# Kernel tuning notes

Measured on AMD Instinct MI355X. Metric: run time of the kernel, lower is better.

Reference implementation:

```python
import jax, jax.numpy as jnp
import numpy as np

N_NODES = 100000
N_EDGES = 1200000
N_FEAT = 128
HIDDEN = 64
N_CLASSES = 40


def setup_inputs() -> dict:
    key = jax.random.key(0)
    k1, k2, k3, k4 = jax.random.split(key, 4)
    x = jax.random.normal(k1, (N_NODES, N_FEAT), dtype=jnp.float32)
    edge_index = jax.random.randint(k2, (2, N_EDGES), 0, N_NODES, dtype=jnp.int64)
    # Glorot-style init for the linear weights (as in PyG GCNConv)
    W1 = jax.random.normal(k3, (N_FEAT, HIDDEN), dtype=jnp.float32) * (1.0 / np.sqrt(N_FEAT))
    b1 = jnp.zeros((HIDDEN,), dtype=jnp.float32)
    W2 = jax.random.normal(k4, (HIDDEN, N_CLASSES), dtype=jnp.float32) * (1.0 / np.sqrt(HIDDEN))
    b2 = jnp.zeros((N_CLASSES,), dtype=jnp.float32)
    return {"x": x, "edge_index": edge_index, "W1": W1, "b1": b1, "W2": W2, "b2": b2}


def _gcn_conv(x, row, col, dinv, W, b):
    # x: [N, Fin], W: [Fin, Fout]. Transform then normalized scatter-add aggregation.
    h = x @ W                                  # [N, Fout]
    norm = dinv[row] * dinv[col]               # [E'] symmetric normalization
    msgs = h[row] * norm[:, None]              # [E', Fout] gather + scale
    out = jax.ops.segment_sum(msgs, col, num_segments=x.shape[0])  # scatter-add
    return out + b


def reference(x, edge_index, W1, b1, W2, b2):
    N = x.shape[0]
    loops = jnp.arange(N, dtype=edge_index.dtype)
    # add self loops (PyG GCNConv default)
    row = jnp.concatenate([edge_index[0], loops])
    col = jnp.concatenate([edge_index[1], loops])
    deg = jax.ops.segment_sum(jnp.ones_like(col, dtype=x.dtype), col, num_segments=N)
    dinv = jax.lax.rsqrt(deg)  # deg >= 1 thanks to self loops
    h = jax.nn.relu(_gcn_conv(x, row, col, dinv, W1, b1))
    # dropout is identity at inference (training=False)
    return _gcn_conv(h, row, col, dinv, W2, b2)
```

## Files before the change

### kernel.cpp

```cpp
#include <hip/hip_runtime.h>
#include <hip/hip_fp16.h>
#include <type_traits>

#define N_NODES 100000
#define N_EDGES 1200000
#define N_FEAT 128
#define HIDDEN 64
#define N_CLASSES 40

#define BSHIFT 9
#define BMASK 511
#define BUCKET_NODES 512
#define NBK ((N_NODES + BUCKET_NODES - 1) / BUCKET_NODES)
#define BCAP 8192
#define CHUNK 2048

typedef _Float16 f16x8 __attribute__((ext_vector_type(8)));
typedef float f32x4 __attribute__((ext_vector_type(4)));


__global__ __launch_bounds__(256) void bucket_kernel(const int* __restrict__ row,
                                                     const int* __restrict__ col,
                                                     int* __restrict__ gcursor,
                                                     unsigned* __restrict__ bke, int E) {
    __shared__ int hist[NBK];
    __shared__ int pfx[NBK];
    __shared__ int gbase[NBK];
    __shared__ int lcnt[NBK];
    __shared__ unsigned ord[CHUNK];
    __shared__ unsigned char obkt[CHUNK];

    const int t = threadIdx.x;
    const int e0 = blockIdx.x * CHUNK;
    const int nE = min(CHUNK, E - e0);

    for (int i = t; i < NBK; i += 256) {
        hist[i] = 0;
        lcnt[i] = 0;
    }
    __syncthreads();

    for (int i = t; i < nE; i += 256) atomicAdd(&hist[col[e0 + i] >> BSHIFT], 1);
    __syncthreads();

    int v = (t < NBK) ? hist[t] : 0;
    if (t < NBK) pfx[t] = v;
    __syncthreads();
    for (int d = 1; d < 256; d <<= 1) {
        int add = (t >= d && t < NBK) ? pfx[t - d] : 0;
        __syncthreads();
        if (t < NBK) pfx[t] += add;
        __syncthreads();
    }
    if (t < NBK) {
        pfx[t] -= v;
        gbase[t] = t * BCAP + ((v > 0) ? atomicAdd(&gcursor[t], v) : 0);
    }
    __syncthreads();

    for (int i = t; i < nE; i += 256) {
        int r = row[e0 + i];
        int c = col[e0 + i];
        int b = c >> BSHIFT;
        int pos = pfx[b] + atomicAdd(&lcnt[b], 1);
        ord[pos] = ((unsigned)r << BSHIFT) | (unsigned)(c & BMASK);
        obkt[pos] = (unsigned char)b;
    }
    __syncthreads();

    for (int i = t; i < nE; i += 256) {
        int b = obkt[i];
        bke[(size_t)gbase[b] + (i - pfx[b])] = ord[i];
    }
}


__global__ __launch_bounds__(256) void place_kernel(const int* __restrict__ gcursor,
                                                    const unsigned* __restrict__ bke,
                                                    int* __restrict__ rowptr,
                                                    float* __restrict__ dinv,
                                                    int* __restrict__ csr_src, int n) {
    __shared__ int hist[BUCKET_NODES];
    __shared__ int cur[BUCKET_NODES];
    __shared__ int tsum[256];

    const int b = blockIdx.x, t = threadIdx.x;
    const int node0 = b << BSHIFT;
    const int nNodes = min(BUCKET_NODES, n - node0);

    const int myCnt = (t < NBK) ? gcursor[t] : 0;
    tsum[t] = myCnt;
    __syncthreads();
    for (int d = 1; d < 256; d <<= 1) {
        int add = (t >= d) ? tsum[t - d] : 0;
        __syncthreads();
        tsum[t] += add;
        __syncthreads();
    }
    const int base = tsum[b] - gcursor[b];
    const int nb = gcursor[b];
    __syncthreads();

    hist[t] = 0;
    hist[t + 256] = 0;
    __syncthreads();

    const unsigned* src = bke + (size_t)b * BCAP;
    for (int i = t; i < nb; i += 256) atomicAdd(&hist[src[i] & BMASK], 1);
    __syncthreads();

    const int c0 = hist[2 * t];
    const int c1 = hist[2 * t + 1];
    const int s = c0 + c1;
    tsum[t] = s;
    __syncthreads();
    for (int d = 1; d < 256; d <<= 1) {
        int add = (t >= d) ? tsum[t - d] : 0;
        __syncthreads();
        tsum[t] += add;
        __syncthreads();
    }
    const int e0 = base + tsum[t] - s;
    const int e1 = e0 + c0;

    cur[2 * t] = e0;
    cur[2 * t + 1] = e1;
    if (2 * t < nNodes) {
        rowptr[node0 + 2 * t] = e0;
        dinv[node0 + 2 * t] = rsqrtf((float)(c0 + 1));
    }
    if (2 * t + 1 < nNodes) {
        rowptr[node0 + 2 * t + 1] = e1;
        dinv[node0 + 2 * t + 1] = rsqrtf((float)(c1 + 1));
    }
    if (t == 0 && node0 + nNodes == n) rowptr[n] = N_EDGES;
    __syncthreads();

    for (int i = t; i < nb; i += 256) {
        unsigned p = src[i];
        int pos = atomicAdd(&cur[p & BMASK], 1);
        csr_src[pos] = (int)(p >> BSHIFT);
    }
}


template <typename XT, int K, int XSTRIDE, int NOUT, int NOUT_PAD, int OSTRIDE>
__global__ __launch_bounds__(256) void gemm_mfma_kernel(const XT* __restrict__ X,
                                                        const float* __restrict__ W,
                                                        const float* __restrict__ dinv,
                                                        __half* __restrict__ Hs, int M) {
    constexpr int KCH = K / 32;
    constexpr int NT = NOUT_PAD / 16;
    constexpr int WPITCH = NOUT_PAD + 2;

    __shared__ _Float16 wh[K * WPITCH];
    __shared__ float sdinv[256];

    const int tid = threadIdx.x;
    const int bnode0 = blockIdx.x * 256;

    for (int i = tid; i < K * NOUT_PAD; i += 256) {
        int k = i / NOUT_PAD, n = i % NOUT_PAD;
        wh[k * WPITCH + n] = (n < NOUT) ? (_Float16)W[k * NOUT + n] : (_Float16)0.0f;
    }
    {
        int node = bnode0 + tid;
        sdinv[tid] = (node < M) ? dinv[node] : 0.f;
    }
    __syncthreads();

    const int wid = tid >> 6;
    const int lane = tid & 63;
    const int m = lane & 15;
    const int quad = lane >> 4;

    f16x8 bf[KCH][NT];
#pragma unroll
    for (int kc = 0; kc < KCH; ++kc)
#pragma unroll
        for (int nt = 0; nt < NT; ++nt)
#pragma unroll
            for (int j = 0; j < 8; ++j)
                bf[kc][nt][j] = wh[(kc * 32 + quad * 8 + j) * WPITCH + nt * 16 + m];

    for (int nt4 = 0; nt4 < 4; ++nt4) {
        const int nb = bnode0 + wid * 64 + nt4 * 16;
        if (nb >= M) break;
        const int rowi = min(nb + m, M - 1);
        const XT* xr = X + (size_t)rowi * XSTRIDE;

        f32x4 acc[NT];
#pragma unroll
        for (int nt = 0; nt < NT; ++nt) acc[nt] = (f32x4){0.f, 0.f, 0.f, 0.f};

#pragma unroll
        for (int kc = 0; kc < KCH; ++kc) {
            f16x8 af;
            if constexpr (std::is_same<XT, float>::value) {
                float4 u0 = *(const float4*)&xr[kc * 32 + quad * 8];
                float4 u1 = *(const float4*)&xr[kc * 32 + quad * 8 + 4];
                af[0] = (_Float16)u0.x;
                af[1] = (_Float16)u0.y;
                af[2] = (_Float16)u0.z;
                af[3] = (_Float16)u0.w;
                af[4] = (_Float16)u1.x;
                af[5] = (_Float16)u1.y;
                af[6] = (_Float16)u1.z;
                af[7] = (_Float16)u1.w;
            } else {
                af = *(const f16x8*)&xr[kc * 32 + quad * 8];
            }
#pragma unroll
            for (int nt = 0; nt < NT; ++nt)
                acc[nt] = __builtin_amdgcn_mfma_f32_16x16x32_f16(af, bf[kc][nt], acc[nt], 0, 0, 0);
        }

#pragma unroll
        for (int reg = 0; reg < 4; ++reg) {
            const int node = nb + quad * 4 + reg;
            if (node < M) {
                const float s = sdinv[node - bnode0];
#pragma unroll
                for (int nt = 0; nt < NT; ++nt) {
                    const int f = nt * 16 + m;
                    if (NOUT == NOUT_PAD || f < NOUT)
                        Hs[(size_t)node * OSTRIDE + f] = __float2half(acc[nt][reg] * s);
                }
            }
        }
    }
}


__device__ inline void acc_mix16(float (&acc)[8], uint4 u, float one) {
    const unsigned* w = (const unsigned*)&u;
#pragma unroll
    for (int k = 0; k < 4; ++k) {
        asm("v_fma_mix_f32 %0, %1, %2, %0 op_sel:[0,0,0] op_sel_hi:[1,0,0]"
            : "+v"(acc[2 * k])
            : "v"(w[k]), "v"(one));
        asm("v_fma_mix_f32 %0, %1, %2, %0 op_sel:[1,0,0] op_sel_hi:[1,0,0]"
            : "+v"(acc[2 * k + 1])
            : "v"(w[k]), "v"(one));
    }
}


__global__ __launch_bounds__(256) void gather1_gemm2_kernel(
    const int* __restrict__ rowptr, const int* __restrict__ csr_src,
    const float* __restrict__ dinv, const __half* __restrict__ h1s,
    const float* __restrict__ b1, const float* __restrict__ W2,
    __half* __restrict__ h2a, __half* __restrict__ h2b, int n) {
    constexpr int APITCH = 72;
    constexpr int WPITCH = 50;

    __shared__ _Float16 agg[64 * APITCH];
    __shared__ _Float16 wh[64 * WPITCH];
    __shared__ float sdinv[64];

    const int tid = threadIdx.x;
    const int base = blockIdx.x * 64;

    for (int i = tid; i < 64 * 48; i += 256) {
        int k = i / 48, nn = i % 48;
        wh[k * WPITCH + nn] = (nn < 40) ? (_Float16)W2[k * 40 + nn] : (_Float16)0.0f;
    }
    if (tid < 64) {
        int node = base + tid;
        sdinv[tid] = (node < n) ? dinv[node] : 0.f;
    }
    __syncthreads();

    const int wid = tid >> 6;
    const int lane = tid & 63;
    const int g = lane >> 3;
    const int q = lane & 7;
    const float one = 1.0f;
    const __half* hq = h1s + q * 8;

#pragma unroll
    for (int t = 0; t < 2; ++t) {
        const int nl = t * 32 + wid * 8 + g;
        const int c = base + nl;
        if (c < n) {
            float acc[8];
#pragma unroll
            for (int j = 0; j < 8; ++j) acc[j] = 0.f;

            acc_mix16(acc, *(const uint4*)(hq + (size_t)c * HIDDEN), one);

            int e = rowptr[c];
            const int eEnd = rowptr[c + 1];
            for (; e + 2 <= eEnd; e += 2) {
                int r0 = csr_src[e];
                int r1 = csr_src[e + 1];
                uint4 u0 = *(const uint4*)(hq + (size_t)r0 * HIDDEN);
                uint4 u1 = *(const uint4*)(hq + (size_t)r1 * HIDDEN);
                acc_mix16(acc, u0, one);
                acc_mix16(acc, u1, one);
            }
            if (e < eEnd) {
                int r = csr_src[e];
                acc_mix16(acc, *(const uint4*)(hq + (size_t)r * HIDDEN), one);
            }

            const float dc = sdinv[nl];
            _Float16 hv[8];
#pragma unroll
            for (int j = 0; j < 8; ++j) {
                float v = fmaf(acc[j], dc, b1[q * 8 + j]);
                hv[j] = (_Float16)fmaxf(v, 0.f);
            }
            *(f16x8*)&agg[nl * APITCH + q * 8] = *(f16x8*)hv;
        }
    }
    __syncthreads();

    const int m = lane & 15;
    const int quad = lane >> 4;

    f16x8 bf[2][3];
#pragma unroll
    for (int kc = 0; kc < 2; ++kc)
#pragma unroll
        for (int nt = 0; nt < 3; ++nt)
#pragma unroll
            for (int j = 0; j < 8; ++j)
                bf[kc][nt][j] = wh[(kc * 32 + quad * 8 + j) * WPITCH + nt * 16 + m];

    const int nl0 = wid * 16;

    f32x4 acc2[3];
#pragma unroll
    for (int nt = 0; nt < 3; ++nt) acc2[nt] = (f32x4){0.f, 0.f, 0.f, 0.f};

#pragma unroll
    for (int kc = 0; kc < 2; ++kc) {
        f16x8 af = *(const f16x8*)&agg[(nl0 + m) * APITCH + kc * 32 + quad * 8];
#pragma unroll
        for (int nt = 0; nt < 3; ++nt)
            acc2[nt] = __builtin_amdgcn_mfma_f32_16x16x32_f16(af, bf[kc][nt], acc2[nt], 0, 0, 0);
    }

#pragma unroll
    for (int reg = 0; reg < 4; ++reg) {
        const int nl = nl0 + quad * 4 + reg;
        const int node = base + nl;
        if (node < n) {
            const float s = sdinv[nl];
#pragma unroll
            for (int nt = 0; nt < 3; ++nt) {
                const int f = nt * 16 + m;
                const __half hv = __float2half(acc2[nt][reg] * s);
                if (f < 32)
                    h2a[(size_t)node * 32 + f] = hv;
                else if (f < N_CLASSES)
                    h2b[(size_t)node * 8 + (f - 32)] = hv;
            }
        }
    }
}


__global__ __launch_bounds__(256) void gather2_kernel(const int* __restrict__ rowptr,
                                                      const int* __restrict__ csr_src,
                                                      const float* __restrict__ dinv,
                                                      const __half* __restrict__ h2a,
                                                      const __half* __restrict__ h2b,
                                                      const float* __restrict__ bias,
                                                      float* __restrict__ out, int n) {
    const int wave = (blockIdx.x * blockDim.x + threadIdx.x) >> 6;
    const int lane = threadIdx.x & 63;
    if (lane >= 60) return;
    const int g = lane / 5;
    const int q = lane % 5;
    const int c = wave * 12 + g;
    if (c >= n) return;

    const float one = 1.0f;
    const __half* hq = (q < 4) ? (h2a + q * 8) : h2b;
    const int sh = (q < 4) ? 5 : 3;

    const int eBeg = rowptr[c];
    const int eEnd = rowptr[c + 1];

    float acc[8];
#pragma unroll
    for (int j = 0; j < 8; ++j) acc[j] = 0.f;

    acc_mix16(acc, *(const uint4*)(hq + ((size_t)c << sh)), one);

    int e = eBeg;
    for (; e + 2 <= eEnd; e += 2) {
        int r0 = csr_src[e];
        int r1 = csr_src[e + 1];
        uint4 u0 = *(const uint4*)(hq + ((size_t)r0 << sh));
        uint4 u1 = *(const uint4*)(hq + ((size_t)r1 << sh));
        acc_mix16(acc, u0, one);
        acc_mix16(acc, u1, one);
    }
    if (e < eEnd) {
        int r = csr_src[e];
        acc_mix16(acc, *(const uint4*)(hq + ((size_t)r << sh)), one);
    }

    const float dc = dinv[c];
    float o[8];
#pragma unroll
    for (int j = 0; j < 8; ++j) {
        float v = fmaf(acc[j], dc, bias[q * 8 + j]);
        o[j] = v;
    }

    float* dst = &out[(size_t)c * N_CLASSES + q * 8];
    *(float4*)dst = make_float4(o[0], o[1], o[2], o[3]);
    *(float4*)(dst + 4) = make_float4(o[4], o[5], o[6], o[7]);
}


extern "C" void kernel_launch(void* const* d_in, const int* in_sizes, int n_in,
                              void* d_out, int out_size, void* d_ws, size_t ws_size,
                              hipStream_t stream) {
    const float* x = (const float*)d_in[0];
    const int* row = (const int*)d_in[1];
    const int* col = row + N_EDGES;
    const float* W1 = (const float*)d_in[2];
    const float* b1 = (const float*)d_in[3];
    const float* W2 = (const float*)d_in[4];
    const float* b2 = (const float*)d_in[5];
    float* out = (float*)d_out;

    const int N = N_NODES, E = N_EDGES;

    char* p = (char*)d_ws;
    auto alloc = [&](size_t bytes) {
        char* q = p;
        p += (bytes + 255) & ~(size_t)255;
        return q;
    };
    int* rowptr = (int*)alloc((size_t)(N + 1) * 4);
    int* csr_src = (int*)alloc((size_t)E * 4);
    int* gcursor = (int*)alloc((size_t)NBK * 4);
    unsigned* bke = (unsigned*)alloc((size_t)NBK * BCAP * 4);
    float* dinv = (float*)alloc((size_t)N * 4);
    __half* h1s = (__half*)alloc((size_t)N * HIDDEN * 2);
    __half* h2a = (__half*)alloc((size_t)N * 32 * 2);
    __half* h2b = (__half*)alloc((size_t)N * 8 * 2);

    hipMemsetAsync(gcursor, 0, (size_t)NBK * 4, stream);
    bucket_kernel<<<(E + CHUNK - 1) / CHUNK, 256, 0, stream>>>(row, col, gcursor, bke, E);
    place_kernel<<<NBK, 256, 0, stream>>>(gcursor, bke, rowptr, dinv, csr_src, N);

    gemm_mfma_kernel<float, N_FEAT, N_FEAT, HIDDEN, HIDDEN, HIDDEN>
        <<<(N + 255) / 256, 256, 0, stream>>>(x, W1, dinv, h1s, N);

    gather1_gemm2_kernel<<<(N + 63) / 64, 256, 0, stream>>>(rowptr, csr_src, dinv, h1s,
                                                            b1, W2, h2a, h2b, N);

    gather2_kernel<<<(N + 47) / 48, 256, 0, stream>>>(rowptr, csr_src, dinv, h2a, h2b,
                                                      b2, out, N);
}
```

Baseline: 208.9 us.

## Merge edge bucketing and first GEMM into one kernel, move source dinv into gather

The first-layer GEMM no longer depends on dinv, so its blocks are appended to the bucketing kernel's grid and run concurrently with edge bucketing, removing one launch and the serial dependency on place_kernel. To make this possible, the per-source dinv scaling is moved out of the GEMM epilogue into the layer-1 gather, which now loads dinv[r] for every edge and passes it as the FMA multiplier. This trades an extra random 4-byte load per edge for overlap of the two independent phases, and the shared-memory buffer is now sized for the larger of the two roles, which may affect occupancy.

```diff
diff --git a/kernel.cpp b/kernel.cpp
--- a/kernel.cpp
+++ b/kernel.cpp
@@ -14,24 +14,27 @@
 #define NBK ((N_NODES + BUCKET_NODES - 1) / BUCKET_NODES)
 #define BCAP 8192
 #define CHUNK 2048
+#define NCHUNKS ((N_EDGES + CHUNK - 1) / CHUNK)
+#define NT1 ((N_NODES + 255) / 256)
 
 typedef _Float16 f16x8 __attribute__((ext_vector_type(8)));
 typedef float f32x4 __attribute__((ext_vector_type(4)));
 
 
-__global__ __launch_bounds__(256) void bucket_kernel(const int* __restrict__ row,
-                                                     const int* __restrict__ col,
-                                                     int* __restrict__ gcursor,
-                                                     unsigned* __restrict__ bke, int E) {
-    __shared__ int hist[NBK];
-    __shared__ int pfx[NBK];
-    __shared__ int gbase[NBK];
-    __shared__ int lcnt[NBK];
-    __shared__ unsigned ord[CHUNK];
-    __shared__ unsigned char obkt[CHUNK];
+__device__ __forceinline__ void bucket_role(char* smem, const int* __restrict__ row,
+                                            const int* __restrict__ col,
+                                            int* __restrict__ gcursor,
+                                            unsigned* __restrict__ bke, int E,
+                                            int chunk) {
+    int* hist = (int*)smem;
+    int* pfx = hist + NBK;
+    int* gbase = pfx + NBK;
+    int* lcnt = gbase + NBK;
+    unsigned* ord = (unsigned*)(lcnt + NBK);
+    unsigned char* obkt = (unsigned char*)(ord + CHUNK);
 
     const int t = threadIdx.x;
-    const int e0 = blockIdx.x * CHUNK;
+    const int e0 = chunk * CHUNK;
     const int nE = min(CHUNK, E - e0);
 
     for (int i = t; i < NBK; i += 256) {
@@ -72,6 +75,89 @@
         int b = obkt[i];
         bke[(size_t)gbase[b] + (i - pfx[b])] = ord[i];
     }
+}
+
+__device__ __forceinline__ void gemm1_role(char* smem, const float* __restrict__ X,
+                                           const float* __restrict__ W,
+                                           __half* __restrict__ Hs, int M, int bnode0) {
+    constexpr int WPITCH = 66;
+    _Float16* wh = (_Float16*)smem;
+
+    const int tid = threadIdx.x;
+
+    for (int i = tid; i < N_FEAT * HIDDEN; i += 256) {
+        int k = i / HIDDEN, n = i % HIDDEN;
+        wh[k * WPITCH + n] = (_Float16)W[k * HIDDEN + n];
+    }
+    __syncthreads();
+
+    const int wid = tid >> 6;
+    const int lane = tid & 63;
+    const int m = lane & 15;
+    const int quad = lane >> 4;
+
+    f16x8 bf[4][4];
+#pragma unroll
+    for (int kc = 0; kc < 4; ++kc)
+#pragma unroll
+        for (int nt = 0; nt < 4; ++nt)
+#pragma unroll
+            for (int j = 0; j < 8; ++j)
+                bf[kc][nt][j] = wh[(kc * 32 + quad * 8 + j) * WPITCH + nt * 16 + m];
+
+    for (int nt4 = 0; nt4 < 4; ++nt4) {
+        const int nb = bnode0 + wid * 64 + nt4 * 16;
+        if (nb >= M) break;
+        const int rowi = min(nb + m, M - 1);
+        const float* xr = X + (size_t)rowi * N_FEAT;
+
+        f32x4 acc[4];
+#pragma unroll
+        for (int nt = 0; nt < 4; ++nt) acc[nt] = (f32x4){0.f, 0.f, 0.f, 0.f};
+
+#pragma unroll
+        for (int kc = 0; kc < 4; ++kc) {
+            float4 u0 = *(const float4*)&xr[kc * 32 + quad * 8];
+            float4 u1 = *(const float4*)&xr[kc * 32 + quad * 8 + 4];
+            f16x8 af;
+            af[0] = (_Float16)u0.x;
+            af[1] = (_Float16)u0.y;
+            af[2] = (_Float16)u0.z;
+            af[3] = (_Float16)u0.w;
+            af[4] = (_Float16)u1.x;
+            af[5] = (_Float16)u1.y;
+            af[6] = (_Float16)u1.z;
+            af[7] = (_Float16)u1.w;
+#pragma unroll
+            for (int nt = 0; nt < 4; ++nt)
+                acc[nt] = __builtin_amdgcn_mfma_f32_16x16x32_f16(af, bf[kc][nt], acc[nt], 0, 0, 0);
+        }
+
+#pragma unroll
+        for (int reg = 0; reg < 4; ++reg) {
+            const int node = nb + quad * 4 + reg;
+            if (node < M) {
+#pragma unroll
+                for (int nt = 0; nt < 4; ++nt)
+                    Hs[(size_t)node * HIDDEN + nt * 16 + m] = __float2half(acc[nt][reg]);
+            }
+        }
+    }
+}
+
+__global__ __launch_bounds__(256) void k1_bucket_gemm1(const int* __restrict__ row,
+                                                       const int* __restrict__ col,
+                                                       int* __restrict__ gcursor,
+                                                       unsigned* __restrict__ bke, int E,
+                                                       const float* __restrict__ x,
+                                                       const float* __restrict__ W1,
+                                                       __half* __restrict__ h1s, int M) {
+    __shared__ __align__(16) char smem[N_FEAT * 66 * 2];
+    const int bid = blockIdx.x;
+    if (bid < NCHUNKS)
+        bucket_role(smem, row, col, gcursor, bke, E, bid);
+    else
+        gemm1_role(smem, x, W1, h1s, M, (bid - NCHUNKS) * 256);
 }
 
 
@@ -144,104 +230,16 @@
 }
 
 
-template <typename XT, int K, int XSTRIDE, int NOUT, int NOUT_PAD, int OSTRIDE>
-__global__ __launch_bounds__(256) void gemm_mfma_kernel(const XT* __restrict__ X,
-                                                        const float* __restrict__ W,
-                                                        const float* __restrict__ dinv,
-                                                        __half* __restrict__ Hs, int M) {
-    constexpr int KCH = K / 32;
-    constexpr int NT = NOUT_PAD / 16;
-    constexpr int WPITCH = NOUT_PAD + 2;
-
-    __shared__ _Float16 wh[K * WPITCH];
-    __shared__ float sdinv[256];
-
-    const int tid = threadIdx.x;
-    const int bnode0 = blockIdx.x * 256;
-
-    for (int i = tid; i < K * NOUT_PAD; i += 256) {
-        int k = i / NOUT_PAD, n = i % NOUT_PAD;
-        wh[k * WPITCH + n] = (n < NOUT) ? (_Float16)W[k * NOUT + n] : (_Float16)0.0f;
-    }
-    {
-        int node = bnode0 + tid;
-        sdinv[tid] = (node < M) ? dinv[node] : 0.f;
-    }
-    __syncthreads();
-
-    const int wid = tid >> 6;
-    const int lane = tid & 63;
-    const int m = lane & 15;
-    const int quad = lane >> 4;
-
-    f16x8 bf[KCH][NT];
-#pragma unroll
-    for (int kc = 0; kc < KCH; ++kc)
-#pragma unroll
-        for (int nt = 0; nt < NT; ++nt)
-#pragma unroll
-            for (int j = 0; j < 8; ++j)
-                bf[kc][nt][j] = wh[(kc * 32 + quad * 8 + j) * WPITCH + nt * 16 + m];
-
-    for (int nt4 = 0; nt4 < 4; ++nt4) {
-        const int nb = bnode0 + wid * 64 + nt4 * 16;
-        if (nb >= M) break;
-        const int rowi = min(nb + m, M - 1);
-        const XT* xr = X + (size_t)rowi * XSTRIDE;
-
-        f32x4 acc[NT];
-#pragma unroll
-        for (int nt = 0; nt < NT; ++nt) acc[nt] = (f32x4){0.f, 0.f, 0.f, 0.f};
-
-#pragma unroll
-        for (int kc = 0; kc < KCH; ++kc) {
-            f16x8 af;
-            if constexpr (std::is_same<XT, float>::value) {
-                float4 u0 = *(const float4*)&xr[kc * 32 + quad * 8];
-                float4 u1 = *(const float4*)&xr[kc * 32 + quad * 8 + 4];
-                af[0] = (_Float16)u0.x;
-                af[1] = (_Float16)u0.y;
-                af[2] = (_Float16)u0.z;
-                af[3] = (_Float16)u0.w;
-                af[4] = (_Float16)u1.x;
-                af[5] = (_Float16)u1.y;
-                af[6] = (_Float16)u1.z;
-                af[7] = (_Float16)u1.w;
-            } else {
-                af = *(const f16x8*)&xr[kc * 32 + quad * 8];
-            }
-#pragma unroll
-            for (int nt = 0; nt < NT; ++nt)
-                acc[nt] = __builtin_amdgcn_mfma_f32_16x16x32_f16(af, bf[kc][nt], acc[nt], 0, 0, 0);
-        }
-
-#pragma unroll
-        for (int reg = 0; reg < 4; ++reg) {
-            const int node = nb + quad * 4 + reg;
-            if (node < M) {
-                const float s = sdinv[node - bnode0];
-#pragma unroll
-                for (int nt = 0; nt < NT; ++nt) {
-                    const int f = nt * 16 + m;
-                    if (NOUT == NOUT_PAD || f < NOUT)
-                        Hs[(size_t)node * OSTRIDE + f] = __float2half(acc[nt][reg] * s);
-                }
-            }
-        }
-    }
-}
-
-
-__device__ inline void acc_mix16(float (&acc)[8], uint4 u, float one) {
+__device__ inline void acc_mix16(float (&acc)[8], uint4 u, float s) {
     const unsigned* w = (const unsigned*)&u;
 #pragma unroll
     for (int k = 0; k < 4; ++k) {
         asm("v_fma_mix_f32 %0, %1, %2, %0 op_sel:[0,0,0] op_sel_hi:[1,0,0]"
             : "+v"(acc[2 * k])
-            : "v"(w[k]), "v"(one));
+            : "v"(w[k]), "v"(s));
         asm("v_fma_mix_f32 %0, %1, %2, %0 op_sel:[1,0,0] op_sel_hi:[1,0,0]"
             : "+v"(acc[2 * k + 1])
-            : "v"(w[k]), "v"(one));
+            : "v"(w[k]), "v"(s));
     }
 }
 
@@ -275,7 +273,6 @@
     const int lane = tid & 63;
     const int g = lane >> 3;
     const int q = lane & 7;
-    const float one = 1.0f;
     const __half* hq = h1s + q * 8;
 
 #pragma unroll
@@ -287,24 +284,26 @@
 #pragma unroll
             for (int j = 0; j < 8; ++j) acc[j] = 0.f;
 
-            acc_mix16(acc, *(const uint4*)(hq + (size_t)c * HIDDEN), one);
+            const float dc = sdinv[nl];
+            acc_mix16(acc, *(const uint4*)(hq + (size_t)c * HIDDEN), dc);
 
             int e = rowptr[c];
             const int eEnd = rowptr[c + 1];
             for (; e + 2 <= eEnd; e += 2) {
                 int r0 = csr_src[e];
                 int r1 = csr_src[e + 1];
+                float s0 = dinv[r0];
+                float s1 = dinv[r1];
                 uint4 u0 = *(const uint4*)(hq + (size_t)r0 * HIDDEN);
                 uint4 u1 = *(const uint4*)(hq + (size_t)r1 * HIDDEN);
-                acc_mix16(acc, u0, one);
-                acc_mix16(acc, u1, one);
+                acc_mix16(acc, u0, s0);
+                acc_mix16(acc, u1, s1);
             }
             if (e < eEnd) {
                 int r = csr_src[e];
-                acc_mix16(acc, *(const uint4*)(hq + (size_t)r * HIDDEN), one);
+                acc_mix16(acc, *(const uint4*)(hq + (size_t)r * HIDDEN), dinv[r]);
             }
 
-            const float dc = sdinv[nl];
             _Float16 hv[8];
 #pragma unroll
             for (int j = 0; j < 8; ++j) {
@@ -448,11 +447,11 @@
     __half* h2b = (__half*)alloc((size_t)N * 8 * 2);
 
     hipMemsetAsync(gcursor, 0, (size_t)NBK * 4, stream);
-    bucket_kernel<<<(E + CHUNK - 1) / CHUNK, 256, 0, stream>>>(row, col, gcursor, bke, E);
+
+    k1_bucket_gemm1<<<NCHUNKS + NT1, 256, 0, stream>>>(row, col, gcursor, bke, E,
+                                                       x, W1, h1s, N);
+
     place_kernel<<<NBK, 256, 0, stream>>>(gcursor, bke, rowptr, dinv, csr_src, N);
-
-    gemm_mfma_kernel<float, N_FEAT, N_FEAT, HIDDEN, HIDDEN, HIDDEN>
-        <<<(N + 255) / 256, 256, 0, stream>>>(x, W1, dinv, h1s, N);
 
     gather1_gemm2_kernel<<<(N + 63) / 64, 256, 0, stream>>>(rowptr, csr_src, dinv, h1s,
                                                             b1, W2, h2a, h2b, N);
```

After: 205.5 us. No clear change (-1.6%).
